# Kernel optimization log

Hardware: AMD Instinct MI355X
Metric: run time of the kernel (lower is better)

The kernel has to match this reference:

```python
import jax, jax.numpy as jnp
import numpy as np

U, I, D = 100000, 50000, 64
N = U + I
E_G, E_U, E_I = 2400000, 1600000, 800000


def _spmm(rows, cols, vals, x, n):
    # sparse [n, m] @ dense [m, d] via gather + scale + segment-sum scatter
    return jax.ops.segment_sum(x[cols] * vals[:, None], rows, num_segments=n)


def setup_inputs() -> dict:
    key = jax.random.key(0)
    ks = jax.random.split(key, 11)
    return {
        "user_emb": jax.random.normal(ks[0], (U, D), dtype=jnp.float32),
        "item_emb": jax.random.normal(ks[1], (I, D), dtype=jnp.float32),
        "graph_rows": jax.random.randint(ks[2], (E_G,), 0, N, dtype=jnp.int32),
        "graph_cols": jax.random.randint(ks[3], (E_G,), 0, N, dtype=jnp.int32),
        "graph_vals": jax.random.uniform(ks[4], (E_G,), dtype=jnp.float32),
        "user_rows": jax.random.randint(ks[5], (E_U,), 0, U, dtype=jnp.int32),
        "user_cols": jax.random.randint(ks[6], (E_U,), 0, U, dtype=jnp.int32),
        "user_vals": jax.random.uniform(ks[7], (E_U,), dtype=jnp.float32),
        "item_rows": jax.random.randint(ks[8], (E_I,), 0, I, dtype=jnp.int32),
        "item_cols": jax.random.randint(ks[9], (E_I,), 0, I, dtype=jnp.int32),
        "item_vals": jax.random.uniform(ks[10], (E_I,), dtype=jnp.float32),
    }


def reference(user_emb, item_emb,
              graph_rows, graph_cols, graph_vals,
              user_rows, user_cols, user_vals,
              item_rows, item_cols, item_vals):
    all_emb = jnp.concatenate([user_emb, item_emb], axis=0)  # [N, D]
    all_emb1 = _spmm(graph_rows, graph_cols, graph_vals, all_emb, N)
    user_emb2 = _spmm(user_rows, user_cols, user_vals, user_emb, U)
    item_emb2 = _spmm(item_rows, item_cols, item_vals, item_emb, I)
    user_emb1, item_emb1 = all_emb1[:U], all_emb1[U:]
    return (user_emb1, item_emb1, user_emb2, item_emb2)
```

## Files before the change

kernel.cpp:

```cpp
#include <hip/hip_runtime.h>

#define DDIM 64
constexpr int U_CNT = 100000;
constexpr int I_CNT = 50000;
constexpr int N_CNT = U_CNT + I_CNT;
constexpr int NB    = N_CNT + U_CNT + I_CNT;

constexpr int BIN_ROWS_LOG = 8;
constexpr int BIN_ROWS = 1 << BIN_ROWS_LOG;
constexpr int BINS = (NB + BIN_ROWS - 1) / BIN_ROWS;
constexpr int BINS_PAD = 1536;
constexpr int SORT_EDGES = 4096;
constexpr int HIST_EDGES = 16384;
constexpr int CAP = 4672;
constexpr int NSLOT = 10;

constexpr int SB_LOG = 12;
constexpr int NSB = (NB + (1 << SB_LOG) - 1) >> SB_LOG;
constexpr int NSB_PAD = 128;
constexpr int BWIN = 48;

typedef unsigned u32x2 __attribute__((ext_vector_type(2)));
typedef unsigned u32x4 __attribute__((ext_vector_type(4)));

__device__ __forceinline__ int wave_incl_scan(int v, int lane) {
#pragma unroll
    for (int off = 1; off < 64; off <<= 1) {
        int t = __shfl_up(v, off, 64);
        if (lane >= off) v += t;
    }
    return v;
}

__device__ __forceinline__ unsigned short f2bf_rne(float f) {
    unsigned u = __float_as_uint(f);
    unsigned r = (u + 0x7FFFu + ((u >> 16) & 1u)) >> 16;
    return (unsigned short)r;
}

__global__ __launch_bounds__(256) void convert_emb(const float* __restrict__ ue,
                                                   const float* __restrict__ ie,
                                                   unsigned short* __restrict__ emb16) {
    int g = blockIdx.x * 256 + threadIdx.x;
    constexpr int UG = U_CNT * (DDIM / 4);
    constexpr int TG = N_CNT * (DDIM / 4);
    if (g >= TG) return;
    float4 v = (g < UG) ? ((const float4*)ue)[g] : ((const float4*)ie)[g - UG];
    ushort4 o;
    o.x = f2bf_rne(v.x); o.y = f2bf_rne(v.y); o.z = f2bf_rne(v.z); o.w = f2bf_rne(v.w);
    ((ushort4*)emb16)[g] = o;
}

__global__ __launch_bounds__(1024) void hist_conv(const int* __restrict__ gr,
                                                  const int* __restrict__ ur,
                                                  const int* __restrict__ ir,
                                                  int EG, int EU, int EI,
                                                  int* __restrict__ cnt,
                                                  const float* __restrict__ ue,
                                                  const float* __restrict__ ie,
                                                  unsigned short* __restrict__ emb16) {
    __shared__ int h[BINS_PAD];
    for (int i = threadIdx.x; i < BINS_PAD; i += 1024) h[i] = 0;

    if (emb16) {
        constexpr int UG = U_CNT * (DDIM / 4);
        constexpr int TG = N_CNT * (DDIM / 4);
        int stride = (int)gridDim.x * 1024;
        for (int g = blockIdx.x * 1024 + threadIdx.x; g < TG; g += stride) {
            float4 v = (g < UG) ? ((const float4*)ue)[g] : ((const float4*)ie)[g - UG];
            ushort4 o;
            o.x = f2bf_rne(v.x); o.y = f2bf_rne(v.y); o.z = f2bf_rne(v.z); o.w = f2bf_rne(v.w);
            ((ushort4*)emb16)[g] = o;
        }
    }
    __syncthreads();

    int base = blockIdx.x * HIST_EDGES;
    int Et = EG + EU + EI;
    for (int j = 0; j < HIST_EDGES / 1024; ++j) {
        int e = base + j * 1024 + threadIdx.x;
        if (e < Et) {
            int b;
            if (e < EG)           b = gr[e];
            else if (e < EG + EU) b = N_CNT + ur[e - EG];
            else                  b = N_CNT + U_CNT + ir[e - EG - EU];
            atomicAdd(&h[b >> BIN_ROWS_LOG], 1);
        }
    }
    __syncthreads();
    for (int i = threadIdx.x; i < BINS; i += 1024) {
        int v = h[i];
        if (v) atomicAdd(&cnt[i], v);
    }
}

__global__ __launch_bounds__(1024) void scan_bins(const int* __restrict__ cnt,
                                                  int* __restrict__ bin_base,
                                                  int* __restrict__ bin_cursor,
                                                  int* __restrict__ sb_base,
                                                  int* __restrict__ sb_cursor,
                                                  int E_total) {
    __shared__ int wsum[16], woff[16];
    int tid = threadIdx.x, lane = tid & 63, wid = tid >> 6;
    int i0 = 2 * tid, i1 = 2 * tid + 1;
    int c0 = (i0 < BINS) ? cnt[i0] : 0;
    int c1 = (i1 < BINS) ? cnt[i1] : 0;
    int v = c0 + c1;
    int incl = wave_incl_scan(v, lane);
    if (lane == 63) wsum[wid] = incl;
    __syncthreads();
    if (wid == 0 && lane < 16) {
        int s = wsum[lane], si = s;
#pragma unroll
        for (int off = 1; off < 16; off <<= 1) {
            int t = __shfl_up(si, off, 64);
            if (lane >= off) si += t;
        }
        woff[lane] = si - s;
    }
    __syncthreads();
    int e = incl - v + woff[wid];
    if (i0 < BINS) { bin_base[i0] = e;      bin_cursor[i0] = e; }
    if (i1 < BINS) { bin_base[i1] = e + c0; bin_cursor[i1] = e + c0; }
    if (tid == 0) bin_base[BINS] = E_total;
    if (sb_base) {
        __syncthreads();
        if (tid <= NSB) {
            int idx = tid << (SB_LOG - BIN_ROWS_LOG);
            int vv = (idx >= BINS) ? E_total : bin_base[idx];
            sb_base[tid] = vv;
            if (tid < NSB) sb_cursor[tid] = vv;
        }
    }
}

__global__ __launch_bounds__(512, 6) void sbsort_all(
        const int* __restrict__ gr, const int* __restrict__ gc, const float* __restrict__ gv,
        const int* __restrict__ ur, const int* __restrict__ uc, const float* __restrict__ uv,
        const int* __restrict__ ir, const int* __restrict__ ic, const float* __restrict__ iv,
        int EG, int EU, int EI,
        int* __restrict__ sb_cursor, uint2* __restrict__ poolA) {
    __shared__ uint2 sorted[SORT_EDGES];
    __shared__ unsigned char ssb[SORT_EDGES];
    __shared__ int hist[NSB_PAD];
    __shared__ int lscan[NSB_PAD];
    __shared__ int lcur[NSB_PAD];
    __shared__ int wsum2[2];

    int tid = threadIdx.x, lane = tid & 63, wid = tid >> 6;
    for (int i = tid; i < NSB_PAD; i += 512) { hist[i] = 0; lcur[i] = 0; }
    __syncthreads();

    const int Et = EG + EU + EI;
    int start = blockIdx.x * SORT_EDGES;
    int base_e = start + tid * 8;
    int myb[8]; unsigned mylo[8]; float myv[8];

#pragma unroll
    for (int j = 0; j < 8; j += 4) {
        int e = base_e + j;
        int sg0 = (e < EG) ? 0 : (e < EG + EU ? 1 : 2);
        int sg3 = (e + 3 < EG) ? 0 : (e + 3 < EG + EU ? 1 : 2);
        if (e + 3 < Et && sg0 == sg3) {
            const int* R; const int* Cc; const float* V; int boff, goff, loc;
            if (sg0 == 0)      { R = gr; Cc = gc; V = gv; boff = 0;             goff = 0;     loc = e; }
            else if (sg0 == 1) { R = ur; Cc = uc; V = uv; boff = N_CNT;         goff = 0;     loc = e - EG; }
            else               { R = ir; Cc = ic; V = iv; boff = N_CNT + U_CNT; goff = U_CNT; loc = e - EG - EU; }
            int4   r4 = *(const int4*)(R + loc);
            int4   c4 = *(const int4*)(Cc + loc);
            float4 v4 = *(const float4*)(V + loc);
            int rr[4] = {r4.x, r4.y, r4.z, r4.w};
            int cc[4] = {c4.x, c4.y, c4.z, c4.w};
            float vv[4] = {v4.x, v4.y, v4.z, v4.w};
#pragma unroll
            for (int q = 0; q < 4; ++q) {
                int bucket = boff + rr[q];
                int sb = bucket >> SB_LOG;
                myb[j + q] = sb;
                mylo[j + q] = ((unsigned)(bucket & 4095) << 18) | (unsigned)(goff + cc[q]);
                myv[j + q] = vv[q];
                atomicAdd(&hist[sb], 1);
            }
        } else {
#pragma unroll
            for (int q = 0; q < 4; ++q) {
                int ee = e + q;
                if (ee < Et) {
                    int r, c; float vl; int boff, goff;
                    if (ee < EG)           { r = gr[ee]; c = gc[ee]; vl = gv[ee]; boff = 0; goff = 0; }
                    else if (ee < EG + EU) { int k = ee - EG;      r = ur[k]; c = uc[k]; vl = uv[k]; boff = N_CNT;         goff = 0; }
                    else                   { int k = ee - EG - EU; r = ir[k]; c = ic[k]; vl = iv[k]; boff = N_CNT + U_CNT; goff = U_CNT; }
                    int bucket = boff + r;
                    int sb = bucket >> SB_LOG;
                    myb[j + q] = sb;
                    mylo[j + q] = ((unsigned)(bucket & 4095) << 18) | (unsigned)(goff + c);
                    myv[j + q] = vl;
                    atomicAdd(&hist[sb], 1);
                } else myb[j + q] = -1;
            }
        }
    }
    __syncthreads();

    int v = 0, incl = 0;
    if (tid < NSB_PAD) {
        v = hist[tid];
        incl = wave_incl_scan(v, lane);
        if (lane == 63) wsum2[wid] = incl;
    }
    __syncthreads();
    if (tid < NSB_PAD) {
        int st = incl - v + (wid ? wsum2[0] : 0);
        lscan[tid] = st;
        if (tid < NSB && v) hist[tid] = atomicAdd(&sb_cursor[tid], v);
    }
    __syncthreads();

#pragma unroll
    for (int j = 0; j < 8; ++j) {
        if (myb[j] >= 0) {
            int p = lscan[myb[j]] + atomicAdd(&lcur[myb[j]], 1);
            sorted[p] = make_uint2(mylo[j], __float_as_uint(myv[j]));
            ssb[p] = (unsigned char)myb[j];
        }
    }
    __syncthreads();

    int cntE = min(SORT_EDGES, Et - start);
    for (int pos = tid; pos < cntE; pos += 512) {
        int b = ssb[pos];
        uint2 t = sorted[pos];
        u32x2 q; q.x = t.x; q.y = t.y;
        __builtin_nontemporal_store(q, (u32x2*)&poolA[hist[b] + (pos - lscan[b])]);
    }
}

__global__ __launch_bounds__(512, 6) void binsort2(const uint2* __restrict__ poolA,
                                                   const int* __restrict__ sb_base, int Et,
                                                   int* __restrict__ bin_cursor,
                                                   uint2* __restrict__ poolB) {
    __shared__ uint2 sorted[SORT_EDGES];
    __shared__ unsigned char sbin[SORT_EDGES];
    __shared__ int hist[BWIN];
    __shared__ int lscan[BWIN];
    __shared__ int lcur[BWIN];
    __shared__ int ssbb[NSB + 1];
    __shared__ int W0s, nloc;

    int tid = threadIdx.x, lane = tid & 63;
    if (tid < BWIN) { hist[tid] = 0; }
    if (tid <= NSB) ssbb[tid] = sb_base[tid];
    __syncthreads();

    int start = blockIdx.x * SORT_EDGES;
    int base_e = start + tid * 8;
    int sb;
    {
        int lo2 = 0, hi2 = NSB - 1;
        while (lo2 < hi2) {
            int mid = (lo2 + hi2 + 1) >> 1;
            if (ssbb[mid] <= base_e) lo2 = mid; else hi2 = mid - 1;
        }
        sb = lo2;
    }
    if (tid == 0) W0s = sb << (SB_LOG - BIN_ROWS_LOG);
    __syncthreads();
    int W0 = W0s;

    int myb[8]; uint2 myp[8];
#pragma unroll
    for (int j = 0; j < 8; j += 2) {
        int e = base_e + j;
        uint2 p0, p1;
        bool v1 = (e + 1 < Et), v0 = (e < Et);
        if (v1) {
            u32x4 q = __builtin_nontemporal_load((const u32x4*)(poolA + e));
            p0.x = q.x; p0.y = q.y; p1.x = q.z; p1.y = q.w;
        } else if (v0) {
            u32x2 q = __builtin_nontemporal_load((const u32x2*)(poolA + e));
            p0.x = q.x; p0.y = q.y;
        }
        if (v0) {
            while (sb < NSB - 1 && e >= ssbb[sb + 1]) ++sb;
            int b = (sb << (SB_LOG - BIN_ROWS_LOG)) + (int)(p0.x >> 26);
            int slot = b - W0;
            if ((unsigned)slot < (unsigned)BWIN) {
                myb[j] = slot; myp[j] = p0;
                atomicAdd(&hist[slot], 1);
            } else {
                int gp = atomicAdd(&bin_cursor[b], 1);
                poolB[gp] = p0;
                myb[j] = -1;
            }
        } else myb[j] = -1;
        if (v1) {
            int e1 = e + 1;
            while (sb < NSB - 1 && e1 >= ssbb[sb + 1]) ++sb;
            int b = (sb << (SB_LOG - BIN_ROWS_LOG)) + (int)(p1.x >> 26);
            int slot = b - W0;
            if ((unsigned)slot < (unsigned)BWIN) {
                myb[j + 1] = slot; myp[j + 1] = p1;
                atomicAdd(&hist[slot], 1);
            } else {
                int gp = atomicAdd(&bin_cursor[b], 1);
                poolB[gp] = p1;
                myb[j + 1] = -1;
            }
        } else myb[j + 1] = -1;
    }
    __syncthreads();

    if (tid < 64) {
        int vv = (tid < BWIN) ? hist[tid] : 0;
        int incl = wave_incl_scan(vv, lane);
        if (tid < BWIN) { lscan[tid] = incl - vv; lcur[tid] = incl - vv; }
        if (tid == BWIN - 1) nloc = incl;
    }
    __syncthreads();
    if (tid < BWIN && hist[tid] > 0)
        hist[tid] = atomicAdd(&bin_cursor[W0 + tid], hist[tid]);
    __syncthreads();

#pragma unroll
    for (int j = 0; j < 8; ++j) {
        if (myb[j] >= 0) {
            int p = atomicAdd(&lcur[myb[j]], 1);
            sorted[p] = myp[j];
            sbin[p] = (unsigned char)myb[j];
        }
    }
    __syncthreads();

    int tot = nloc;
    for (int pos = tid; pos < tot; pos += 512) {
        int sl = sbin[pos];
        uint2 t = sorted[pos];
        u32x2 q; q.x = t.x; q.y = t.y;
        __builtin_nontemporal_store(q, (u32x2*)&poolB[hist[sl] + (pos - lscan[sl])]);
    }
}

__global__ __launch_bounds__(512) void binsort(const int* __restrict__ rows,
                                               const int* __restrict__ cols,
                                               const float* __restrict__ vals, int E,
                                               int bucket_base, int gidx_base,
                                               int* __restrict__ bin_cursor,
                                               uint2* __restrict__ pool) {
    __shared__ uint2 sorted[SORT_EDGES];
    __shared__ unsigned short sbin[SORT_EDGES];
    __shared__ int hist[BINS_PAD];
    __shared__ int lscan[BINS_PAD];
    __shared__ int lcur[BINS_PAD];
    __shared__ int wsum[8], woff[8];

    int tid = threadIdx.x, lane = tid & 63, wid = tid >> 6;
    for (int i = tid; i < BINS_PAD; i += 512) { hist[i] = 0; lcur[i] = 0; }
    __syncthreads();

    int start = blockIdx.x * SORT_EDGES;
    int base_e = start + tid * 8;
    int myb[8]; unsigned mylo[8]; float myv[8];
#pragma unroll
    for (int j = 0; j < 8; j += 4) {
        int e = base_e + j;
        if (e + 3 < E) {
            int4   r4 = *(const int4*)(rows + e);
            int4   c4 = *(const int4*)(cols + e);
            float4 v4 = *(const float4*)(vals + e);
            int rr[4] = {r4.x, r4.y, r4.z, r4.w};
            int cc[4] = {c4.x, c4.y, c4.z, c4.w};
            float vv[4] = {v4.x, v4.y, v4.z, v4.w};
#pragma unroll
            for (int q = 0; q < 4; ++q) {
                int bucket = bucket_base + rr[q];
                myb[j + q] = bucket >> BIN_ROWS_LOG;
                mylo[j + q] = ((unsigned)(bucket & (BIN_ROWS - 1)) << 18) |
                              (unsigned)(gidx_base + cc[q]);
                myv[j + q] = vv[q];
                atomicAdd(&hist[myb[j + q]], 1);
            }
        } else {
#pragma unroll
            for (int q = 0; q < 4; ++q) {
                int ee = e + q;
                if (ee < E) {
                    int bucket = bucket_base + rows[ee];
                    myb[j + q] = bucket >> BIN_ROWS_LOG;
                    mylo[j + q] = ((unsigned)(bucket & (BIN_ROWS - 1)) << 18) |
                                  (unsigned)(gidx_base + cols[ee]);
                    myv[j + q] = vals[ee];
                    atomicAdd(&hist[myb[j + q]], 1);
                } else myb[j + q] = -1;
            }
        }
    }
    __syncthreads();

    int s0 = 3 * tid, s1 = s0 + 1, s2 = s0 + 2;
    int h0 = hist[s0], h1 = hist[s1], h2 = hist[s2];
    int v = h0 + h1 + h2;
    int incl = wave_incl_scan(v, lane);
    if (lane == 63) wsum[wid] = incl;
    __syncthreads();
    if (wid == 0 && lane < 8) {
        int s = wsum[lane], si = s;
#pragma unroll
        for (int off = 1; off < 8; off <<= 1) {
            int t = __shfl_up(si, off, 64);
            if (lane >= off) si += t;
        }
        woff[lane] = si - s;
    }
    __syncthreads();
    int e0 = incl - v + woff[wid];
    lscan[s0] = e0; lscan[s1] = e0 + h0; lscan[s2] = e0 + h0 + h1;
    if (s0 < BINS && h0) hist[s0] = atomicAdd(&bin_cursor[s0], h0);
    if (s1 < BINS && h1) hist[s1] = atomicAdd(&bin_cursor[s1], h1);
    if (s2 < BINS && h2) hist[s2] = atomicAdd(&bin_cursor[s2], h2);
    __syncthreads();

#pragma unroll
    for (int j = 0; j < 8; ++j) {
        if (myb[j] >= 0) {
            int p = lscan[myb[j]] + atomicAdd(&lcur[myb[j]], 1);
            sorted[p] = make_uint2(mylo[j], __float_as_uint(myv[j]));
            sbin[p] = (unsigned short)myb[j];
        }
    }
    __syncthreads();

    int cntE = min(SORT_EDGES, E - start);
    for (int pos = tid; pos < cntE; pos += 512) {
        int b = sbin[pos];
        pool[hist[b] + (pos - lscan[b])] = sorted[pos];
    }
}

template <bool BF16>
__global__ __launch_bounds__(512, 8) void refine_accum(const int* __restrict__ bin_base,
                                                       const uint2* __restrict__ pool,
                                                       const unsigned short* __restrict__ emb16,
                                                       const float* __restrict__ ue,
                                                       const float* __restrict__ ie,
                                                       float* __restrict__ out) {
    __shared__ uint2 sorted[CAP];
    __shared__ int rhist[BIN_ROWS];
    __shared__ int rstart[BIN_ROWS];
    __shared__ int rcur[BIN_ROWS];
    __shared__ int wsum[4];
    int tid = threadIdx.x, lane = tid & 63, wid = tid >> 6;
    int b = blockIdx.x;
    int s = bin_base[b], e = bin_base[b + 1];
    int cnt = min(e - s, CAP);

    if (tid < BIN_ROWS) rhist[tid] = 0;
    __syncthreads();

    uint2 my[NSLOT];
    const u32x2* poolv = (const u32x2*)(pool + s);
#pragma unroll
    for (int j = 0; j < NSLOT; ++j) {
        int idx = tid + j * 512;
        if (idx < cnt) {
            u32x2 q = __builtin_nontemporal_load(poolv + idx);
            my[j].x = q.x; my[j].y = q.y;
            atomicAdd(&rhist[(q.x >> 18) & 255u], 1);
        }
    }
    __syncthreads();

    int v = 0, incl = 0;
    if (tid < BIN_ROWS) {
        v = rhist[tid];
        incl = wave_incl_scan(v, lane);
        if (lane == 63) wsum[wid] = incl;
    }
    __syncthreads();
    if (tid < BIN_ROWS) {
        int off = 0;
#pragma unroll
        for (int w = 0; w < 4; ++w)
            if (w < wid) off += wsum[w];
        int st = incl - v + off;
        rstart[tid] = st; rcur[tid] = st;
    }
    __syncthreads();

#pragma unroll
    for (int j = 0; j < NSLOT; ++j) {
        int idx = tid + j * 512;
        if (idx < cnt) {
            int pos = atomicAdd(&rcur[(my[j].x >> 18) & 255u], 1);
            sorted[pos] = my[j];
        }
    }
    __syncthreads();

    long long rowbase = (long long)b * BIN_ROWS;
    auto gather = [&](unsigned gi) -> float {
        if (BF16) return __uint_as_float((unsigned)emb16[(gi << 6) + lane] << 16);
        return (gi < (unsigned)U_CNT) ? ue[((size_t)gi << 6) + lane]
                                      : ie[(((size_t)gi - U_CNT) << 6) + lane];
    };
    for (int r = wid; r < BIN_ROWS; r += 8) {
        long long row = rowbase + r;
        if (row >= NB) break;
        int k = rstart[r], ke = k + rhist[r];
        float acc0 = 0.f, acc1 = 0.f;
        for (; k + 8 <= ke; k += 8) {
            uint2 p0 = sorted[k],     p1 = sorted[k + 1], p2 = sorted[k + 2], p3 = sorted[k + 3];
            uint2 p4 = sorted[k + 4], p5 = sorted[k + 5], p6 = sorted[k + 6], p7 = sorted[k + 7];
            float x0 = gather(p0.x & 0x3FFFFu);
            float x1 = gather(p1.x & 0x3FFFFu);
            float x2 = gather(p2.x & 0x3FFFFu);
            float x3 = gather(p3.x & 0x3FFFFu);
            float x4 = gather(p4.x & 0x3FFFFu);
            float x5 = gather(p5.x & 0x3FFFFu);
            float x6 = gather(p6.x & 0x3FFFFu);
            float x7 = gather(p7.x & 0x3FFFFu);
            acc0 += __uint_as_float(p0.y) * x0;
            acc1 += __uint_as_float(p1.y) * x1;
            acc0 += __uint_as_float(p2.y) * x2;
            acc1 += __uint_as_float(p3.y) * x3;
            acc0 += __uint_as_float(p4.y) * x4;
            acc1 += __uint_as_float(p5.y) * x5;
            acc0 += __uint_as_float(p6.y) * x6;
            acc1 += __uint_as_float(p7.y) * x7;
        }
        for (; k + 4 <= ke; k += 4) {
            uint2 p0 = sorted[k], p1 = sorted[k + 1], p2 = sorted[k + 2], p3 = sorted[k + 3];
            float x0 = gather(p0.x & 0x3FFFFu);
            float x1 = gather(p1.x & 0x3FFFFu);
            float x2 = gather(p2.x & 0x3FFFFu);
            float x3 = gather(p3.x & 0x3FFFFu);
            acc0 += __uint_as_float(p0.y) * x0;
            acc1 += __uint_as_float(p1.y) * x1;
            acc0 += __uint_as_float(p2.y) * x2;
            acc1 += __uint_as_float(p3.y) * x3;
        }
        for (; k < ke; ++k) {
            uint2 p = sorted[k];
            acc0 += __uint_as_float(p.y) * gather(p.x & 0x3FFFFu);
        }
        __builtin_nontemporal_store(acc0 + acc1, &out[(size_t)row * DDIM + lane]);
    }
}

__global__ void spmm_graph_kernel(const int* __restrict__ rows, const int* __restrict__ cols,
                                  const float* __restrict__ vals,
                                  const float* __restrict__ user_emb,
                                  const float* __restrict__ item_emb,
                                  float* __restrict__ out, int E) {
    long long idx = (long long)blockIdx.x * blockDim.x + threadIdx.x;
    int e = (int)(idx >> 6), d = (int)(idx & 63);
    if (e >= E) return;
    int r = rows[e], c = cols[e];
    float v = vals[e];
    float x = (c < U_CNT) ? user_emb[(long long)c * DDIM + d]
                          : item_emb[(long long)(c - U_CNT) * DDIM + d];
    atomicAdd(&out[(long long)r * DDIM + d], v * x);
}

__global__ void spmm_plain_kernel(const int* __restrict__ rows, const int* __restrict__ cols,
                                  const float* __restrict__ vals,
                                  const float* __restrict__ emb,
                                  float* __restrict__ out, int E) {
    long long idx = (long long)blockIdx.x * blockDim.x + threadIdx.x;
    int e = (int)(idx >> 6), d = (int)(idx & 63);
    if (e >= E) return;
    int r = rows[e], c = cols[e];
    atomicAdd(&out[(long long)r * DDIM + d], vals[e] * emb[(long long)c * DDIM + d]);
}

extern "C" void kernel_launch(void* const* d_in, const int* in_sizes, int n_in,
                              void* d_out, int out_size, void* d_ws, size_t ws_size,
                              hipStream_t stream) {
    const float* user_emb = (const float*)d_in[0];
    const float* item_emb = (const float*)d_in[1];
    const int*   g_rows   = (const int*)d_in[2];
    const int*   g_cols   = (const int*)d_in[3];
    const float* g_vals   = (const float*)d_in[4];
    const int*   u_rows   = (const int*)d_in[5];
    const int*   u_cols   = (const int*)d_in[6];
    const float* u_vals   = (const float*)d_in[7];
    const int*   i_rows   = (const int*)d_in[8];
    const int*   i_cols   = (const int*)d_in[9];
    const float* i_vals   = (const float*)d_in[10];
    float* out = (float*)d_out;

    const int EG = in_sizes[2];
    const int EU = in_sizes[5];
    const int EI = in_sizes[8];
    const int Et = EG + EU + EI;

    const size_t emb_bytes = (size_t)N_CNT * DDIM * sizeof(unsigned short);

    size_t t_off_bb   = (size_t)BINS_PAD * sizeof(int);
    size_t t_off_bc   = t_off_bb + (size_t)(BINS + 1) * sizeof(int);
    size_t t_off_sbb  = t_off_bc + (size_t)BINS * sizeof(int);
    size_t t_off_sbc  = t_off_sbb + (size_t)(NSB + 1) * sizeof(int);
    size_t t_off_pa   = (t_off_sbc + (size_t)NSB * sizeof(int) + 15) & ~(size_t)15;
    size_t t_off_pb   = t_off_pa + (size_t)Et * sizeof(uint2);
    size_t needed_2p  = t_off_pb + (size_t)Et * sizeof(uint2);
    size_t t_off_emb  = (needed_2p + 15) & ~(size_t)15;
    size_t needed_na  = t_off_emb + emb_bytes;
    bool pa_fits_emb  = (size_t)Et * sizeof(uint2) >= emb_bytes;

    size_t o_off_base   = (size_t)BINS_PAD * sizeof(int);
    size_t o_off_cursor = o_off_base + (size_t)(BINS + 1) * sizeof(int);
    size_t o_off_pool   = (o_off_cursor + (size_t)BINS * sizeof(int) + 15) & ~(size_t)15;
    size_t o_off_emb    = o_off_pool + (size_t)Et * sizeof(uint2);
    size_t needed_min   = o_off_emb;
    size_t needed_full  = o_off_emb + emb_bytes;

    if (ws_size >= needed_2p && pa_fits_emb) {
        bool noalias = (ws_size >= needed_na);
        int*   cnt        = (int*)d_ws;
        int*   bin_base   = (int*)((char*)d_ws + t_off_bb);
        int*   bin_cursor = (int*)((char*)d_ws + t_off_bc);
        int*   sb_base    = (int*)((char*)d_ws + t_off_sbb);
        int*   sb_cursor  = (int*)((char*)d_ws + t_off_sbc);
        uint2* poolA      = (uint2*)((char*)d_ws + t_off_pa);
        uint2* poolB      = (uint2*)((char*)d_ws + t_off_pb);
        unsigned short* emb16 = noalias ? (unsigned short*)((char*)d_ws + t_off_emb)
                                        : (unsigned short*)poolA;

        hipMemsetAsync(cnt, 0, (size_t)BINS_PAD * sizeof(int), stream);

        unsigned hblocks = (unsigned)((Et + HIST_EDGES - 1) / HIST_EDGES);
        hist_conv<<<hblocks, 1024, 0, stream>>>(g_rows, u_rows, i_rows, EG, EU, EI, cnt,
                                                user_emb, item_emb,
                                                noalias ? emb16 : (unsigned short*)nullptr);
        scan_bins<<<1, 1024, 0, stream>>>(cnt, bin_base, bin_cursor, sb_base, sb_cursor, Et);

        unsigned nb2 = (unsigned)((Et + SORT_EDGES - 1) / SORT_EDGES);
        sbsort_all<<<nb2, 512, 0, stream>>>(g_rows, g_cols, g_vals,
                                            u_rows, u_cols, u_vals,
                                            i_rows, i_cols, i_vals,
                                            EG, EU, EI, sb_cursor, poolA);
        binsort2<<<nb2, 512, 0, stream>>>(poolA, sb_base, Et, bin_cursor, poolB);

        if (!noalias) {
            unsigned cgrid = (unsigned)((N_CNT * (DDIM / 4) + 255) / 256);
            convert_emb<<<cgrid, 256, 0, stream>>>(user_emb, item_emb, emb16);
        }

        refine_accum<true><<<BINS, 512, 0, stream>>>(bin_base, poolB, emb16,
                                                     user_emb, item_emb, out);
    } else if (ws_size >= needed_min) {
        int*   cnt        = (int*)d_ws;
        int*   bin_base   = (int*)((char*)d_ws + o_off_base);
        int*   bin_cursor = (int*)((char*)d_ws + o_off_cursor);
        uint2* pool       = (uint2*)((char*)d_ws + o_off_pool);
        unsigned short* emb16 = (unsigned short*)((char*)d_ws + o_off_emb);
        bool use_bf16 = (ws_size >= needed_full);

        hipMemsetAsync(cnt, 0, (size_t)BINS_PAD * sizeof(int), stream);

        unsigned hblocks = (unsigned)((Et + HIST_EDGES - 1) / HIST_EDGES);
        hist_conv<<<hblocks, 1024, 0, stream>>>(g_rows, u_rows, i_rows, EG, EU, EI, cnt,
                                                user_emb, item_emb,
                                                use_bf16 ? emb16 : (unsigned short*)nullptr);
        scan_bins<<<1, 1024, 0, stream>>>(cnt, bin_base, bin_cursor, nullptr, nullptr, Et);

        unsigned gb = (unsigned)((EG + SORT_EDGES - 1) / SORT_EDGES);
        unsigned ub = (unsigned)((EU + SORT_EDGES - 1) / SORT_EDGES);
        unsigned ib = (unsigned)((EI + SORT_EDGES - 1) / SORT_EDGES);
        binsort<<<gb, 512, 0, stream>>>(g_rows, g_cols, g_vals, EG, 0,             0,     bin_cursor, pool);
        binsort<<<ub, 512, 0, stream>>>(u_rows, u_cols, u_vals, EU, N_CNT,         0,     bin_cursor, pool);
        binsort<<<ib, 512, 0, stream>>>(i_rows, i_cols, i_vals, EI, N_CNT + U_CNT, U_CNT, bin_cursor, pool);

        if (use_bf16)
            refine_accum<true><<<BINS, 512, 0, stream>>>(bin_base, pool, emb16,
                                                         user_emb, item_emb, out);
        else
            refine_accum<false><<<BINS, 512, 0, stream>>>(bin_base, pool, (const unsigned short*)nullptr,
                                                          user_emb, item_emb, out);
    } else {
        hipMemsetAsync(d_out, 0, (size_t)out_size * sizeof(float), stream);
        const int block = 256;
        {
            long long t = (long long)EG * DDIM;
            spmm_graph_kernel<<<(unsigned)((t + block - 1) / block), block, 0, stream>>>(
                g_rows, g_cols, g_vals, user_emb, item_emb, out, EG);
        }
        {
            long long t = (long long)EU * DDIM;
            spmm_plain_kernel<<<(unsigned)((t + block - 1) / block), block, 0, stream>>>(
                u_rows, u_cols, u_vals, user_emb, out + (size_t)N_CNT * DDIM, EU);
        }
        {
            long long t = (long long)EI * DDIM;
            spmm_plain_kernel<<<(unsigned)((t + block - 1) / block), block, 0, stream>>>(
                i_rows, i_cols, i_vals, item_emb, out + (size_t)(N_CNT + U_CNT) * DDIM, EI);
        }
    }
}
```

Before: 357.0 us.

## Interleave two rows per wave in bin SpMM, raise sort occupancy, align pools

The per-bin SpMM loop now processes two rows per wavefront at once, issuing 16 independent embedding gathers per iteration to raise memory-level parallelism, then drains the leftovers of each row separately. The two sort kernels request 8 waves per SIMD instead of 6 through launch bounds, which may force register spilling. Workspace pool offsets are aligned to 128 bytes instead of 16. The wider unroll raises register pressure in the SpMM kernel and could lower its occupancy.

```diff
diff --git a/kernel.cpp b/kernel.cpp
--- a/kernel.cpp
+++ b/kernel.cpp
@@ -134,7 +134,7 @@
     }
 }
 
-__global__ __launch_bounds__(512, 6) void sbsort_all(
+__global__ __launch_bounds__(512, 8) void sbsort_all(
         const int* __restrict__ gr, const int* __restrict__ gc, const float* __restrict__ gv,
         const int* __restrict__ ur, const int* __restrict__ uc, const float* __restrict__ uv,
         const int* __restrict__ ir, const int* __restrict__ ic, const float* __restrict__ iv,
@@ -235,7 +235,7 @@
     }
 }
 
-__global__ __launch_bounds__(512, 6) void binsort2(const uint2* __restrict__ poolA,
+__global__ __launch_bounds__(512, 8) void binsort2(const uint2* __restrict__ poolA,
                                                    const int* __restrict__ sb_base, int Et,
                                                    int* __restrict__ bin_cursor,
                                                    uint2* __restrict__ poolB) {
@@ -502,11 +502,7 @@
         return (gi < (unsigned)U_CNT) ? ue[((size_t)gi << 6) + lane]
                                       : ie[(((size_t)gi - U_CNT) << 6) + lane];
     };
-    for (int r = wid; r < BIN_ROWS; r += 8) {
-        long long row = rowbase + r;
-        if (row >= NB) break;
-        int k = rstart[r], ke = k + rhist[r];
-        float acc0 = 0.f, acc1 = 0.f;
+    auto drain = [&](int k, int ke, float& c0, float& c1) {
         for (; k + 8 <= ke; k += 8) {
             uint2 p0 = sorted[k],     p1 = sorted[k + 1], p2 = sorted[k + 2], p3 = sorted[k + 3];
             uint2 p4 = sorted[k + 4], p5 = sorted[k + 5], p6 = sorted[k + 6], p7 = sorted[k + 7];
@@ -518,14 +514,14 @@
             float x5 = gather(p5.x & 0x3FFFFu);
             float x6 = gather(p6.x & 0x3FFFFu);
             float x7 = gather(p7.x & 0x3FFFFu);
-            acc0 += __uint_as_float(p0.y) * x0;
-            acc1 += __uint_as_float(p1.y) * x1;
-            acc0 += __uint_as_float(p2.y) * x2;
-            acc1 += __uint_as_float(p3.y) * x3;
-            acc0 += __uint_as_float(p4.y) * x4;
-            acc1 += __uint_as_float(p5.y) * x5;
-            acc0 += __uint_as_float(p6.y) * x6;
-            acc1 += __uint_as_float(p7.y) * x7;
+            c0 += __uint_as_float(p0.y) * x0;
+            c1 += __uint_as_float(p1.y) * x1;
+            c0 += __uint_as_float(p2.y) * x2;
+            c1 += __uint_as_float(p3.y) * x3;
+            c0 += __uint_as_float(p4.y) * x4;
+            c1 += __uint_as_float(p5.y) * x5;
+            c0 += __uint_as_float(p6.y) * x6;
+            c1 += __uint_as_float(p7.y) * x7;
         }
         for (; k + 4 <= ke; k += 4) {
             uint2 p0 = sorted[k], p1 = sorted[k + 1], p2 = sorted[k + 2], p3 = sorted[k + 3];
@@ -533,16 +529,51 @@
             float x1 = gather(p1.x & 0x3FFFFu);
             float x2 = gather(p2.x & 0x3FFFFu);
             float x3 = gather(p3.x & 0x3FFFFu);
-            acc0 += __uint_as_float(p0.y) * x0;
-            acc1 += __uint_as_float(p1.y) * x1;
-            acc0 += __uint_as_float(p2.y) * x2;
-            acc1 += __uint_as_float(p3.y) * x3;
+            c0 += __uint_as_float(p0.y) * x0;
+            c1 += __uint_as_float(p1.y) * x1;
+            c0 += __uint_as_float(p2.y) * x2;
+            c1 += __uint_as_float(p3.y) * x3;
         }
         for (; k < ke; ++k) {
             uint2 p = sorted[k];
-            acc0 += __uint_as_float(p.y) * gather(p.x & 0x3FFFFu);
-        }
-        __builtin_nontemporal_store(acc0 + acc1, &out[(size_t)row * DDIM + lane]);
+            c0 += __uint_as_float(p.y) * gather(p.x & 0x3FFFFu);
+        }
+    };
+
+    for (int r = wid; r < BIN_ROWS; r += 16) {
+        int r2 = r + 8;
+        long long row1 = rowbase + r;
+        long long row2 = rowbase + r2;
+        bool has1 = (row1 < NB);
+        bool has2 = (r2 < BIN_ROWS) && (row2 < NB);
+        int k1 = 0, ke1 = 0, k2 = 0, ke2 = 0;
+        if (has1) { k1 = rstart[r];  ke1 = k1 + rhist[r]; }
+        if (has2) { k2 = rstart[r2]; ke2 = k2 + rhist[r2]; }
+        float a0 = 0.f, a1 = 0.f, b0 = 0.f, b1 = 0.f;
+        while (k1 + 8 <= ke1 && k2 + 8 <= ke2) {
+            uint2 p[16]; float x[16];
+#pragma unroll
+            for (int j = 0; j < 8; ++j) p[j] = sorted[k1 + j];
+#pragma unroll
+            for (int j = 0; j < 8; ++j) p[8 + j] = sorted[k2 + j];
+#pragma unroll
+            for (int j = 0; j < 16; ++j) x[j] = gather(p[j].x & 0x3FFFFu);
+#pragma unroll
+            for (int j = 0; j < 8; j += 2) {
+                a0 += __uint_as_float(p[j].y) * x[j];
+                a1 += __uint_as_float(p[j + 1].y) * x[j + 1];
+            }
+#pragma unroll
+            for (int j = 8; j < 16; j += 2) {
+                b0 += __uint_as_float(p[j].y) * x[j];
+                b1 += __uint_as_float(p[j + 1].y) * x[j + 1];
+            }
+            k1 += 8; k2 += 8;
+        }
+        drain(k1, ke1, a0, a1);
+        drain(k2, ke2, b0, b1);
+        if (has1) __builtin_nontemporal_store(a0 + a1, &out[(size_t)row1 * DDIM + lane]);
+        if (has2) __builtin_nontemporal_store(b0 + b1, &out[(size_t)row2 * DDIM + lane]);
     }
 }
 
@@ -599,17 +630,17 @@
     size_t t_off_bc   = t_off_bb + (size_t)(BINS + 1) * sizeof(int);
     size_t t_off_sbb  = t_off_bc + (size_t)BINS * sizeof(int);
     size_t t_off_sbc  = t_off_sbb + (size_t)(NSB + 1) * sizeof(int);
-    size_t t_off_pa   = (t_off_sbc + (size_t)NSB * sizeof(int) + 15) & ~(size_t)15;
-    size_t t_off_pb   = t_off_pa + (size_t)Et * sizeof(uint2);
+    size_t t_off_pa   = (t_off_sbc + (size_t)NSB * sizeof(int) + 127) & ~(size_t)127;
+    size_t t_off_pb   = (t_off_pa + (size_t)Et * sizeof(uint2) + 127) & ~(size_t)127;
     size_t needed_2p  = t_off_pb + (size_t)Et * sizeof(uint2);
-    size_t t_off_emb  = (needed_2p + 15) & ~(size_t)15;
+    size_t t_off_emb  = (needed_2p + 127) & ~(size_t)127;
     size_t needed_na  = t_off_emb + emb_bytes;
     bool pa_fits_emb  = (size_t)Et * sizeof(uint2) >= emb_bytes;
 
     size_t o_off_base   = (size_t)BINS_PAD * sizeof(int);
     size_t o_off_cursor = o_off_base + (size_t)(BINS + 1) * sizeof(int);
-    size_t o_off_pool   = (o_off_cursor + (size_t)BINS * sizeof(int) + 15) & ~(size_t)15;
-    size_t o_off_emb    = o_off_pool + (size_t)Et * sizeof(uint2);
+    size_t o_off_pool   = (o_off_cursor + (size_t)BINS * sizeof(int) + 127) & ~(size_t)127;
+    size_t o_off_emb    = (o_off_pool + (size_t)Et * sizeof(uint2) + 127) & ~(size_t)127;
     size_t needed_min   = o_off_emb;
     size_t needed_full  = o_off_emb + emb_bytes;
 
```

After: 355.8 us. No clear change (-0.3%).
